# Optimization experiments

Measured on AMD Instinct MI355X. Metric: run time of the kernel, lower is better.

The kernel has to match this reference:

```python
import jax, jax.numpy as jnp
import numpy as np

DIM = 1024
HEADS = 16
HEAD_DIM = 64
INNER = HEADS * HEAD_DIM  # 1024
B, N = 4, 2048
EPS = 1e-5


def setup_inputs() -> dict:
    key = jax.random.key(0)
    ks = jax.random.split(key, 5)
    x = jax.random.normal(ks[0], (B, N, DIM), dtype=jnp.float32)
    w_qkv = jax.random.normal(ks[1], (DIM, 3 * INNER), dtype=jnp.float32) * (DIM ** -0.5)
    w_out = jax.random.normal(ks[2], (INNER, DIM), dtype=jnp.float32) * (INNER ** -0.5)
    b_out = jax.random.normal(ks[3], (DIM,), dtype=jnp.float32) * 0.01
    ln_gamma = jnp.ones((DIM,), dtype=jnp.float32)
    ln_beta = jnp.zeros((DIM,), dtype=jnp.float32)
    return {"x": x, "w_qkv": w_qkv, "w_out": w_out, "b_out": b_out,
            "ln_gamma": ln_gamma, "ln_beta": ln_beta}


def reference(x, w_qkv, w_out, b_out, ln_gamma, ln_beta):
    scale = HEAD_DIM ** -0.5
    qkv = x @ w_qkv  # [b, n, 3*inner]
    q, k, v = jnp.split(qkv, 3, axis=-1)
    q = q * scale
    # [b, n, h*d] -> [b, h, n, d]
    def to_heads(t):
        b, n, _ = t.shape
        return t.reshape(b, n, HEADS, HEAD_DIM).transpose(0, 2, 1, 3)
    q, k, v = to_heads(q), to_heads(k), to_heads(v)
    scores = jnp.einsum('bhid,bhjd->bhij', q, k)
    attn = jax.nn.softmax(scores, axis=-1)  # max-subtraction (detached) is internal
    out = jnp.einsum('bhij,bhjd->bhid', attn, v)
    out = out.transpose(0, 2, 1, 3).reshape(x.shape[0], x.shape[1], INNER)
    out = out @ w_out + b_out
    # LayerNorm over last dim
    mu = out.mean(axis=-1, keepdims=True)
    var = out.var(axis=-1, keepdims=True)
    out = (out - mu) * jax.lax.rsqrt(var + EPS)
    return out * ln_gamma + ln_beta
```

## Files before the change

### kernel.cpp

```cpp
#include <hip/hip_runtime.h>


typedef __bf16 bf16;
typedef __bf16 bf16x4 __attribute__((ext_vector_type(4)));
typedef __bf16 bf16x8 __attribute__((ext_vector_type(8)));
typedef float f32x4 __attribute__((ext_vector_type(4)));
typedef float f32x16 __attribute__((ext_vector_type(16)));
typedef unsigned int u32x2 __attribute__((ext_vector_type(2)));
typedef unsigned int u32x4 __attribute__((ext_vector_type(4)));

#define QSCALE_LOG2E 0.18033688011112042f

#define GLOAD_LDS16(gp, lp)                                                   \
  __builtin_amdgcn_global_load_lds(                                           \
      (const __attribute__((address_space(1))) unsigned int*)(const void*)(gp), \
      (__attribute__((address_space(3))) unsigned int*)(void*)(lp), 16, 0, 0)

__device__ __forceinline__ float fexp2(float x) {
#if __has_builtin(__builtin_amdgcn_exp2f)
  return __builtin_amdgcn_exp2f(x);
#else
  return __expf(x * 0.6931471805599453f);
#endif
}

__device__ __forceinline__ unsigned pack2t(float lo, float hi) {
  return __builtin_amdgcn_perm(__float_as_uint(hi), __float_as_uint(lo), 0x07060302u);
}

__global__ __launch_bounds__(256) void cvt_k(const float* __restrict__ in,
                                             bf16* __restrict__ out) {
  const size_t i = ((size_t)blockIdx.x * 256 + threadIdx.x) * 8;
  float4 a = *(const float4*)(in + i);
  float4 b = *(const float4*)(in + i + 4);
  bf16x8 o = {(bf16)a.x, (bf16)a.y, (bf16)a.z, (bf16)a.w,
              (bf16)b.x, (bf16)b.y, (bf16)b.z, (bf16)b.w};
  *(bf16x8*)(out + i) = o;
}

__global__ __launch_bounds__(256) void transpose_k(const float* __restrict__ in,
                                                   bf16* __restrict__ out,
                                                   int Kd, int Nd) {
  __shared__ bf16 t[32][36];
  const int n0 = blockIdx.x * 32, k0 = blockIdx.y * 32;
  const int r = threadIdx.x >> 3, c4 = (threadIdx.x & 7) * 4;
  float4 v = *(const float4*)(in + (size_t)(k0 + r) * Nd + n0 + c4);
  t[c4 + 0][r] = (bf16)v.x; t[c4 + 1][r] = (bf16)v.y;
  t[c4 + 2][r] = (bf16)v.z; t[c4 + 3][r] = (bf16)v.w;
  __syncthreads();
  bf16x4 o = *(const bf16x4*)&t[r][c4];
  *(bf16x4*)(out + (size_t)(n0 + r) * Kd + k0 + c4) = o;
}

template <bool QKV>
__global__ __launch_bounds__(256) void gemm2(const bf16* __restrict__ A,
                                             const bf16* __restrict__ Bt,
                                             bf16* __restrict__ C,
                                             bf16* __restrict__ Vt) {
  __shared__ bf16 As[3][128][32];
  __shared__ bf16 Bs[3][128][32];
  const int tid = threadIdx.x;
  const int l = tid & 63, w = tid >> 6;
  const int g = l >> 4, q = l & 15;
  const int wm = w >> 1, wn = w & 1;
  const int m0 = blockIdx.x * 128, n0 = blockIdx.y * 128;
  const int lr = l >> 2, lc = (l & 3) * 8;

  f32x4 acc[4][4] = {};

#define GSTAGE(buf, k0)                                                         \
  do {                                                                          \
    _Pragma("unroll")                                                           \
    for (int i = 0; i < 2; i++) {                                               \
      const int c = w + i * 4;                                                  \
      GLOAD_LDS16(A + (size_t)(m0 + c * 16 + lr) * 1024 + (k0) + lc,            \
                  &As[buf][c * 16][0]);                                         \
      GLOAD_LDS16(Bt + (size_t)(n0 + c * 16 + lr) * 1024 + (k0) + lc,           \
                  &Bs[buf][c * 16][0]);                                         \
    }                                                                           \
  } while (0)

  GSTAGE(0, 0);
  GSTAGE(1, 32);
  int cur = 0, nxt2 = 2;

  for (int k0 = 0; k0 < 1024; k0 += 32) {
    if (k0 == 992) {
      asm volatile("s_waitcnt vmcnt(0)" ::: "memory");
    } else {
      asm volatile("s_waitcnt vmcnt(4)" ::: "memory");
    }
    __builtin_amdgcn_sched_barrier(0);
    __builtin_amdgcn_s_barrier();

    if (k0 + 64 < 1024) GSTAGE(nxt2, k0 + 64);

    bf16x8 af[4], bfr[4];
#pragma unroll
    for (int mi = 0; mi < 4; mi++)
      af[mi] = *(const bf16x8*)&As[cur][wm * 64 + mi * 16 + q][g * 8];
#pragma unroll
    for (int ni = 0; ni < 4; ni++)
      bfr[ni] = *(const bf16x8*)&Bs[cur][wn * 64 + ni * 16 + q][g * 8];
#pragma unroll
    for (int mi = 0; mi < 4; mi++)
#pragma unroll
      for (int ni = 0; ni < 4; ni++)
        acc[mi][ni] = __builtin_amdgcn_mfma_f32_16x16x32_bf16(af[mi], bfr[ni], acc[mi][ni], 0, 0, 0);

    cur = (cur == 2) ? 0 : cur + 1;
    nxt2 = (nxt2 == 2) ? 0 : nxt2 + 1;
  }

  if (QKV && n0 >= 2048) {
#pragma unroll
    for (int mi = 0; mi < 4; mi++)
#pragma unroll
      for (int ni = 0; ni < 4; ni++) {
        const int vcol = n0 - 2048 + wn * 64 + ni * 16 + q;
        const int h = vcol >> 6, d = vcol & 63;
        const int t0 = m0 + wm * 64 + mi * 16 + g * 4;
        const int b = t0 >> 11, n = t0 & 2047;
        bf16x4 o = {(bf16)acc[mi][ni][0], (bf16)acc[mi][ni][1],
                    (bf16)acc[mi][ni][2], (bf16)acc[mi][ni][3]};
        *(bf16x4*)(Vt + ((size_t)(b * 16 + h) * 64 + d) * 2048 + n) = o;
      }
  } else {
    const int ldc = QKV ? 2048 : 1024;
    const float s = (QKV && n0 < 1024) ? QSCALE_LOG2E : 1.0f;
#pragma unroll
    for (int mi = 0; mi < 4; mi++)
#pragma unroll
      for (int ni = 0; ni < 4; ni++) {
        const int col = n0 + wn * 64 + ni * 16 + q;
#pragma unroll
        for (int r = 0; r < 4; r++) {
          const int row = m0 + wm * 64 + mi * 16 + g * 4 + r;
          C[(size_t)row * ldc + col] = (bf16)(acc[mi][ni][r] * s);
        }
      }
  }
#undef GSTAGE
}

__global__ __launch_bounds__(256, 3) void attn_k(const bf16* __restrict__ qk,
                                                 const bf16* __restrict__ vt,
                                                 bf16* __restrict__ aout) {
  __shared__ bf16 Ks[3][64][64];
  __shared__ bf16 Vs[3][64][64];
  const int tid = threadIdx.x;
  const int l = tid & 63, w = tid >> 6;
  const int q = l & 31, hi = l >> 5, q7 = q & 7;

  const int flat = blockIdx.x;
  const int logical = (flat & 7) * 128 + (flat >> 3);
  const int qt = logical & 15, bh = logical >> 4;
  const int h = bh & 15, b = bh >> 4;
  const int qbase = qt * 128 + w * 32;

  const bf16* Kg = qk + (size_t)(b * 2048) * 2048 + 1024 + h * 64;
  const bf16* Vg = vt + ((size_t)(b * 16 + h) * 64) * 2048;

  bf16x8 qf[4];
  {
    const bf16* Qr = qk + (size_t)(b * 2048 + qbase + q) * 2048 + h * 64 + hi * 8;
#pragma unroll
    for (int i = 0; i < 4; i++) qf[i] = *(const bf16x8*)(Qr + i * 16);
  }

  const int r0 = tid >> 3, sp0 = ((tid & 7) ^ (r0 & 7)) * 8;
  const int ub = (tid >> 6) << 9;
#define STAGE_KV(buf, kt)                                                       \
  do {                                                                          \
    bf16* kd = &Ks[buf][0][0];                                                  \
    bf16* vd = &Vs[buf][0][0];                                                  \
    GLOAD_LDS16(Kg + (size_t)((kt) + r0) * 2048 + sp0, kd + ub);                \
    GLOAD_LDS16(Vg + (size_t)r0 * 2048 + (kt) + sp0, vd + ub);                  \
    GLOAD_LDS16(Kg + (size_t)((kt) + 32 + r0) * 2048 + sp0, kd + 2048 + ub);    \
    GLOAD_LDS16(Vg + (size_t)(32 + r0) * 2048 + (kt) + sp0, vd + 2048 + ub);    \
  } while (0)

#define QKT(buf, sA, sB)                                                        \
  do {                                                                          \
    const char* Kb_ = (const char*)&Ks[buf][0][0];                              \
    __builtin_amdgcn_s_setprio(1);                                              \
    {                                                                           \
      f32x16 a_ = {};                                                           \
      _Pragma("unroll")                                                         \
      for (int i = 0; i < 4; i++) {                                             \
        bf16x8 kf = *(const bf16x8*)(Kb_ + q * 128 + (((2 * i + hi) ^ q7) << 4));\
        a_ = __builtin_amdgcn_mfma_f32_32x32x16_bf16(kf, qf[i], a_, 0, 0, 0);   \
      }                                                                         \
      sA = a_;                                                                  \
    }                                                                           \
    {                                                                           \
      f32x16 a_ = {};                                                           \
      _Pragma("unroll")                                                         \
      for (int i = 0; i < 4; i++) {                                             \
        bf16x8 kf = *(const bf16x8*)(Kb_ + (32 + q) * 128 +                     \
                                     (((2 * i + hi) ^ q7) << 4));               \
        a_ = __builtin_amdgcn_mfma_f32_32x32x16_bf16(kf, qf[i], a_, 0, 0, 0);   \
      }                                                                         \
      sB = a_;                                                                  \
    }                                                                           \
    __builtin_amdgcn_s_setprio(0);                                              \
  } while (0)

  f32x16 oacc[2] = {};
  float lsA = 0.f, lsB = 0.f;

  STAGE_KV(0, 0);
  STAGE_KV(1, 64);
  asm volatile("s_waitcnt vmcnt(4)" ::: "memory");
  __builtin_amdgcn_sched_barrier(0);
  __builtin_amdgcn_s_barrier();

  f32x16 s0, s1;
  QKT(0, s0, s1);

  int cur = 0;
  for (int kt = 0; kt < 2048; kt += 64) {
    const int nbuf = (cur == 2) ? 0 : cur + 1;
    const int sbuf = (nbuf == 2) ? 0 : nbuf + 1;

    asm volatile("s_waitcnt vmcnt(0)" ::: "memory");
    __builtin_amdgcn_sched_barrier(0);
    __builtin_amdgcn_s_barrier();

    if (kt + 128 < 2048) STAGE_KV(sbuf, kt + 128);

    f32x16 n0v, n1v;
    QKT(nbuf, n0v, n1v);

#pragma unroll
    for (int r = 0; r < 16; r++) { s0[r] = fexp2(s0[r]); lsA += s0[r]; }
#pragma unroll
    for (int r = 0; r < 16; r++) { s1[r] = fexp2(s1[r]); lsB += s1[r]; }

    bf16x8 pfrag[4];
#pragma unroll
    for (int ks = 0; ks < 2; ks++) {
      const unsigned a0 = pack2t(s0[8 * ks + 0], s0[8 * ks + 1]);
      const unsigned a1 = pack2t(s0[8 * ks + 2], s0[8 * ks + 3]);
      const unsigned b0 = pack2t(s0[8 * ks + 4], s0[8 * ks + 5]);
      const unsigned b1 = pack2t(s0[8 * ks + 6], s0[8 * ks + 7]);
      u32x2 w0 = __builtin_amdgcn_permlane32_swap(a0, b0, false, false);
      u32x2 w1 = __builtin_amdgcn_permlane32_swap(a1, b1, false, false);
      u32x4 bw = {w0[0], w1[0], w0[1], w1[1]};
      pfrag[ks] = __builtin_bit_cast(bf16x8, bw);
    }
#pragma unroll
    for (int ks = 0; ks < 2; ks++) {
      const unsigned a0 = pack2t(s1[8 * ks + 0], s1[8 * ks + 1]);
      const unsigned a1 = pack2t(s1[8 * ks + 2], s1[8 * ks + 3]);
      const unsigned b0 = pack2t(s1[8 * ks + 4], s1[8 * ks + 5]);
      const unsigned b1 = pack2t(s1[8 * ks + 6], s1[8 * ks + 7]);
      u32x2 w0 = __builtin_amdgcn_permlane32_swap(a0, b0, false, false);
      u32x2 w1 = __builtin_amdgcn_permlane32_swap(a1, b1, false, false);
      u32x4 bw = {w0[0], w1[0], w0[1], w1[1]};
      pfrag[2 + ks] = __builtin_bit_cast(bf16x8, bw);
    }

    const char* Vb = (const char*)&Vs[cur][0][0];
    __builtin_amdgcn_s_setprio(1);
#pragma unroll
    for (int dblk = 0; dblk < 2; dblk++) {
      bf16x8 vfr[4];
#pragma unroll
      for (int t = 0; t < 4; t++)
        vfr[t] = *(const bf16x8*)(Vb + (dblk * 32 + q) * 128 + (((2 * t + hi) ^ q7) << 4));
#pragma unroll
      for (int t = 0; t < 4; t++)
        oacc[dblk] = __builtin_amdgcn_mfma_f32_32x32x16_bf16(vfr[t], pfrag[t],
                                                             oacc[dblk], 0, 0, 0);
    }
    __builtin_amdgcn_s_setprio(0);

    s0 = n0v; s1 = n1v;
    cur = nbuf;
  }

  float lsum = lsA + lsB;
  {
    u32x2 t2 = __builtin_amdgcn_permlane32_swap(__float_as_uint(lsum),
                                                __float_as_uint(lsum), false, false);
    lsum = __uint_as_float(t2[0]) + __uint_as_float(t2[1]);
  }
  const float inv = 1.f / lsum;
  bf16* orow = aout + (size_t)(b * 2048 + qbase + q) * 1024 + h * 64 + hi * 4;
#pragma unroll
  for (int dblk = 0; dblk < 2; dblk++)
#pragma unroll
    for (int rg = 0; rg < 4; rg++) {
      bf16x4 o = {(bf16)(oacc[dblk][4 * rg + 0] * inv), (bf16)(oacc[dblk][4 * rg + 1] * inv),
                  (bf16)(oacc[dblk][4 * rg + 2] * inv), (bf16)(oacc[dblk][4 * rg + 3] * inv)};
      *(bf16x4*)(orow + dblk * 32 + rg * 8) = o;
    }
#undef QKT
#undef STAGE_KV
}

__global__ __launch_bounds__(256) void ln_k(const bf16* __restrict__ proj,
                                            const float* __restrict__ bo,
                                            const float* __restrict__ gam,
                                            const float* __restrict__ bet,
                                            float* __restrict__ out) {
  const int tid = threadIdx.x;
  const int l = tid & 63, w = tid >> 6;
  const int row = blockIdx.x * 4 + w;
  const int c0 = l * 16;

  bf16x8 p0 = *(const bf16x8*)(proj + (size_t)row * 1024 + c0);
  bf16x8 p1 = *(const bf16x8*)(proj + (size_t)row * 1024 + c0 + 8);
  float v[16];
#pragma unroll
  for (int j = 0; j < 8; j++) { v[j] = (float)p0[j]; v[8 + j] = (float)p1[j]; }
#pragma unroll
  for (int j = 0; j < 4; j++) {
    float4 bv = *(const float4*)(bo + c0 + j * 4);
    v[4 * j + 0] += bv.x; v[4 * j + 1] += bv.y;
    v[4 * j + 2] += bv.z; v[4 * j + 3] += bv.w;
  }
  float s = 0.f, ss = 0.f;
#pragma unroll
  for (int j = 0; j < 16; j++) { s += v[j]; ss += v[j] * v[j]; }
#pragma unroll
  for (int off = 32; off > 0; off >>= 1) {
    s += __shfl_xor(s, off);
    ss += __shfl_xor(ss, off);
  }
  const float mean = s * (1.f / 1024.f);
  const float var = ss * (1.f / 1024.f) - mean * mean;
  const float rs = rsqrtf(var + 1e-5f);
#pragma unroll
  for (int j = 0; j < 4; j++) {
    float4 gv = *(const float4*)(gam + c0 + j * 4);
    float4 btv = *(const float4*)(bet + c0 + j * 4);
    float4 o;
    o.x = (v[4 * j + 0] - mean) * rs * gv.x + btv.x;
    o.y = (v[4 * j + 1] - mean) * rs * gv.y + btv.y;
    o.z = (v[4 * j + 2] - mean) * rs * gv.z + btv.z;
    o.w = (v[4 * j + 3] - mean) * rs * gv.w + btv.w;
    *(float4*)(out + (size_t)row * 1024 + c0 + j * 4) = o;
  }
}

extern "C" void kernel_launch(void* const* d_in, const int* in_sizes, int n_in,
                              void* d_out, int out_size, void* d_ws, size_t ws_size,
                              hipStream_t stream) {
  const float* x      = (const float*)d_in[0];
  const float* w_qkv  = (const float*)d_in[1];
  const float* w_out  = (const float*)d_in[2];
  const float* b_out  = (const float*)d_in[3];
  const float* gamma  = (const float*)d_in[4];
  const float* beta   = (const float*)d_in[5];
  float* out = (float*)d_out;

  char* ws = (char*)d_ws;
  bf16* xbf   = (bf16*)(ws);
  bf16* wqkvT = (bf16*)(ws + 16777216);
  bf16* woutT = (bf16*)(ws + 23068672);
  bf16* qkbuf = (bf16*)(ws + 25165824);
  bf16* vt    = (bf16*)(ws + 58720256);
  bf16* aout  = xbf;
  bf16* proj  = vt;

  dim3 blk(256);
  cvt_k<<<4096, blk, 0, stream>>>(x, xbf);
  transpose_k<<<dim3(96, 32), blk, 0, stream>>>(w_qkv, wqkvT, 1024, 3072);
  transpose_k<<<dim3(32, 32), blk, 0, stream>>>(w_out, woutT, 1024, 1024);
  gemm2<true><<<dim3(64, 24), blk, 0, stream>>>(xbf, wqkvT, qkbuf, vt);
  attn_k<<<1024, blk, 0, stream>>>(qkbuf, vt, aout);
  gemm2<false><<<dim3(64, 8), blk, 0, stream>>>(aout, woutT, proj, nullptr);
  ln_k<<<2048, blk, 0, stream>>>(proj, b_out, gamma, beta, out);
}
```

Measured before the change: 208.1 us.

## Merge prep kernels into one launch and drop GEMM triple-buffer pipeline

Folds the x conversion and both weight transposes into a single prep kernel indexed by block id, which removes two kernel launches. The GEMM's three-stage async LDS pipeline with explicit vmcnt waits is replaced by a single-buffer loop that loads a tile, synchronizes, and computes. That cuts LDS use and may raise occupancy, but global loads no longer overlap with MFMA work, so the GEMMs risk stalling on memory latency.

```diff
diff --git a/kernel.cpp b/kernel.cpp
--- a/kernel.cpp
+++ b/kernel.cpp
@@ -28,28 +28,42 @@
   return __builtin_amdgcn_perm(__float_as_uint(hi), __float_as_uint(lo), 0x07060302u);
 }
 
-__global__ __launch_bounds__(256) void cvt_k(const float* __restrict__ in,
-                                             bf16* __restrict__ out) {
-  const size_t i = ((size_t)blockIdx.x * 256 + threadIdx.x) * 8;
-  float4 a = *(const float4*)(in + i);
-  float4 b = *(const float4*)(in + i + 4);
-  bf16x8 o = {(bf16)a.x, (bf16)a.y, (bf16)a.z, (bf16)a.w,
-              (bf16)b.x, (bf16)b.y, (bf16)b.z, (bf16)b.w};
-  *(bf16x8*)(out + i) = o;
-}
-
-__global__ __launch_bounds__(256) void transpose_k(const float* __restrict__ in,
-                                                   bf16* __restrict__ out,
-                                                   int Kd, int Nd) {
+__global__ __launch_bounds__(256) void prep_k(const float* __restrict__ x,
+                                              const float* __restrict__ w_qkv,
+                                              const float* __restrict__ w_out,
+                                              bf16* __restrict__ xbf,
+                                              bf16* __restrict__ wqkvT,
+                                              bf16* __restrict__ woutT) {
   __shared__ bf16 t[32][36];
-  const int n0 = blockIdx.x * 32, k0 = blockIdx.y * 32;
+  const int bid = blockIdx.x;
+  if (bid < 4096) {
+    const size_t i = ((size_t)bid * 256 + threadIdx.x) * 8;
+    float4 a = *(const float4*)(x + i);
+    float4 b = *(const float4*)(x + i + 4);
+    bf16x8 o = {(bf16)a.x, (bf16)a.y, (bf16)a.z, (bf16)a.w,
+                (bf16)b.x, (bf16)b.y, (bf16)b.z, (bf16)b.w};
+    *(bf16x8*)(xbf + i) = o;
+    return;
+  }
+  const float* in;
+  bf16* outp;
+  int Kd, Nd, n0, k0;
+  if (bid < 4096 + 3072) {
+    const int idx = bid - 4096;
+    in = w_qkv; outp = wqkvT; Kd = 1024; Nd = 3072;
+    n0 = (idx % 96) * 32; k0 = (idx / 96) * 32;
+  } else {
+    const int idx = bid - 7168;
+    in = w_out; outp = woutT; Kd = 1024; Nd = 1024;
+    n0 = (idx & 31) * 32; k0 = (idx >> 5) * 32;
+  }
   const int r = threadIdx.x >> 3, c4 = (threadIdx.x & 7) * 4;
   float4 v = *(const float4*)(in + (size_t)(k0 + r) * Nd + n0 + c4);
   t[c4 + 0][r] = (bf16)v.x; t[c4 + 1][r] = (bf16)v.y;
   t[c4 + 2][r] = (bf16)v.z; t[c4 + 3][r] = (bf16)v.w;
   __syncthreads();
   bf16x4 o = *(const bf16x4*)&t[r][c4];
-  *(bf16x4*)(out + (size_t)(n0 + r) * Kd + k0 + c4) = o;
+  *(bf16x4*)(outp + (size_t)(n0 + r) * Kd + k0 + c4) = o;
 }
 
 template <bool QKV>
@@ -57,8 +71,8 @@
                                              const bf16* __restrict__ Bt,
                                              bf16* __restrict__ C,
                                              bf16* __restrict__ Vt) {
-  __shared__ bf16 As[3][128][32];
-  __shared__ bf16 Bs[3][128][32];
+  __shared__ bf16 As[128][32];
+  __shared__ bf16 Bs[128][32];
   const int tid = threadIdx.x;
   const int l = tid & 63, w = tid >> 6;
   const int g = l >> 4, q = l & 15;
@@ -68,48 +82,28 @@
 
   f32x4 acc[4][4] = {};
 
-#define GSTAGE(buf, k0)                                                         \
-  do {                                                                          \
-    _Pragma("unroll")                                                           \
-    for (int i = 0; i < 2; i++) {                                               \
-      const int c = w + i * 4;                                                  \
-      GLOAD_LDS16(A + (size_t)(m0 + c * 16 + lr) * 1024 + (k0) + lc,            \
-                  &As[buf][c * 16][0]);                                         \
-      GLOAD_LDS16(Bt + (size_t)(n0 + c * 16 + lr) * 1024 + (k0) + lc,           \
-                  &Bs[buf][c * 16][0]);                                         \
-    }                                                                           \
-  } while (0)
-
-  GSTAGE(0, 0);
-  GSTAGE(1, 32);
-  int cur = 0, nxt2 = 2;
-
   for (int k0 = 0; k0 < 1024; k0 += 32) {
-    if (k0 == 992) {
-      asm volatile("s_waitcnt vmcnt(0)" ::: "memory");
-    } else {
-      asm volatile("s_waitcnt vmcnt(4)" ::: "memory");
-    }
-    __builtin_amdgcn_sched_barrier(0);
-    __builtin_amdgcn_s_barrier();
-
-    if (k0 + 64 < 1024) GSTAGE(nxt2, k0 + 64);
+    __syncthreads();
+#pragma unroll
+    for (int i = 0; i < 2; i++) {
+      const int c = w + i * 4;
+      GLOAD_LDS16(A + (size_t)(m0 + c * 16 + lr) * 1024 + k0 + lc, &As[c * 16][0]);
+      GLOAD_LDS16(Bt + (size_t)(n0 + c * 16 + lr) * 1024 + k0 + lc, &Bs[c * 16][0]);
+    }
+    __syncthreads();
 
     bf16x8 af[4], bfr[4];
 #pragma unroll
     for (int mi = 0; mi < 4; mi++)
-      af[mi] = *(const bf16x8*)&As[cur][wm * 64 + mi * 16 + q][g * 8];
+      af[mi] = *(const bf16x8*)&As[wm * 64 + mi * 16 + q][g * 8];
 #pragma unroll
     for (int ni = 0; ni < 4; ni++)
-      bfr[ni] = *(const bf16x8*)&Bs[cur][wn * 64 + ni * 16 + q][g * 8];
+      bfr[ni] = *(const bf16x8*)&Bs[wn * 64 + ni * 16 + q][g * 8];
 #pragma unroll
     for (int mi = 0; mi < 4; mi++)
 #pragma unroll
       for (int ni = 0; ni < 4; ni++)
         acc[mi][ni] = __builtin_amdgcn_mfma_f32_16x16x32_bf16(af[mi], bfr[ni], acc[mi][ni], 0, 0, 0);
-
-    cur = (cur == 2) ? 0 : cur + 1;
-    nxt2 = (nxt2 == 2) ? 0 : nxt2 + 1;
   }
 
   if (QKV && n0 >= 2048) {
@@ -140,7 +134,6 @@
         }
       }
   }
-#undef GSTAGE
 }
 
 __global__ __launch_bounds__(256, 3) void attn_k(const bf16* __restrict__ qk,
@@ -366,9 +359,7 @@
   bf16* proj  = vt;
 
   dim3 blk(256);
-  cvt_k<<<4096, blk, 0, stream>>>(x, xbf);
-  transpose_k<<<dim3(96, 32), blk, 0, stream>>>(w_qkv, wqkvT, 1024, 3072);
-  transpose_k<<<dim3(32, 32), blk, 0, stream>>>(w_out, woutT, 1024, 1024);
+  prep_k<<<8192, blk, 0, stream>>>(x, w_qkv, w_out, xbf, wqkvT, woutT);
   gemm2<true><<<dim3(64, 24), blk, 0, stream>>>(xbf, wqkvT, qkbuf, vt);
   attn_k<<<1024, blk, 0, stream>>>(qkbuf, vt, aout);
   gemm2<false><<<dim3(64, 8), blk, 0, stream>>>(aout, woutT, proj, nullptr);
```

After: 202.5 us. 1.03x faster.
